# Kernel tuning notes

Hardware: AMD Instinct MI355X
Metric: run time of the kernel (lower is better)

## Reference

```python
import math
import jax, jax.numpy as jnp
import numpy as np

D_MODEL = 1024
D_STATE = 64
BATCH = 8
SEQLEN = 2048


def setup_inputs() -> dict:
    key = jax.random.key(0)
    ks = jax.random.split(key, 8)
    x = jax.random.normal(ks[0], (BATCH, SEQLEN, D_MODEL), dtype=jnp.float32)
    # faithful init: lam_real = -0.5 -> log_Lam_real = log(0.5); Lam_imag = pi*arange(N)
    log_Lam_real = jnp.log(0.5 * jnp.ones((D_STATE,), dtype=jnp.float32))
    Lam_imag = math.pi * jnp.arange(D_STATE, dtype=jnp.float32)
    B_real = 0.02 * jax.random.normal(ks[1], (D_STATE, D_MODEL), dtype=jnp.float32)
    B_imag = 0.02 * jax.random.normal(ks[2], (D_STATE, D_MODEL), dtype=jnp.float32)
    C_real = 0.02 * jax.random.normal(ks[3], (D_MODEL, D_STATE), dtype=jnp.float32)
    C_imag = 0.02 * jax.random.normal(ks[4], (D_MODEL, D_STATE), dtype=jnp.float32)
    Dp = jnp.ones((D_MODEL,), dtype=jnp.float32)
    log_dt = jnp.zeros((1,), dtype=jnp.float32)
    W_out = 0.02 * jax.random.normal(ks[5], (D_MODEL, D_MODEL), dtype=jnp.float32)
    b_out = jnp.zeros((D_MODEL,), dtype=jnp.float32)
    return {"x": x, "log_Lam_real": log_Lam_real, "Lam_imag": Lam_imag,
            "B_real": B_real, "B_imag": B_imag, "C_real": C_real, "C_imag": C_imag,
            "D": Dp, "log_dt": log_dt, "W_out": W_out, "b_out": b_out}


def reference(x, log_Lam_real, Lam_imag, B_real, B_imag, C_real, C_imag, D, log_dt, W_out, b_out):
    B, L, H = x.shape
    N = log_Lam_real.shape[0]
    dt = jnp.exp(log_dt)                          # (1,)
    Lam_r = -jnp.exp(log_Lam_real)                # (N,)
    mag = jnp.exp(Lam_r * dt)                     # (N,)
    Lbar_r = mag * jnp.cos(Lam_imag * dt)         # (N,)
    Lbar_i = mag * jnp.sin(Lam_imag * dt)         # (N,)
    # batched input projection for all timesteps: (B,L,N)
    Bu_r = jnp.einsum('blh,nh->bln', x, dt * B_real)
    Bu_i = jnp.einsum('blh,nh->bln', x, dt * B_imag)

    def step(carry, bu):
        sr, si = carry
        bur, bui = bu
        nr = Lbar_r * sr - Lbar_i * si + bur
        ni = Lbar_r * si + Lbar_i * sr + bui
        return (nr, ni), (nr, ni)

    sr0 = jnp.zeros((B, N), dtype=x.dtype)
    si0 = jnp.zeros((B, N), dtype=x.dtype)
    (sr, si), (SR, SI) = jax.lax.scan(
        step, (sr0, si0),
        (jnp.swapaxes(Bu_r, 0, 1), jnp.swapaxes(Bu_i, 0, 1)))  # scan over L; SR,SI: (L,B,N)
    # output: y_t = Re(C x_t) + D*u_t, vectorized over all t
    y = jnp.einsum('lbn,hn->blh', SR, C_real) - jnp.einsum('lbn,hn->blh', SI, C_imag) + D * x
    out = y @ W_out.T + b_out                     # out_proj (dropout is identity, p=0)
    return out, (sr, si)
```

## Files before the change

### kernel.cpp

```cpp
#include <hip/hip_runtime.h>

#define HD 1024
#define NS 64
#define NB 8
#define LS 2048
#define MT (NB*LS)
#define N2 128
#define KA 1152
#define CHL 16
#define NCH (LS/CHL)
#define NG  (NB*NS)

typedef __attribute__((ext_vector_type(8))) short short8;
typedef __attribute__((ext_vector_type(4))) float f32x4;

#define OB_ABUF 0u
#define OB_BMAT (OB_ABUF + MT*KA*2)
#define OB_BMP  (OB_BMAT + HD*KA*2)
#define OB_BU   (OB_BMP  + N2*HD*2)
#define OB_FR   (OB_BU   + MT*N2*4)
#define OB_FI   (OB_FR   + NG*NCH*4)
#define OB_CR   (OB_FI   + NG*NCH*4)
#define OB_CI   (OB_CR   + NG*NCH*4)
#define OB_WB   (OB_CI   + NG*NCH*4)
#define OB_CCT  (OB_WB   + HD*HD*2)

__device__ __forceinline__ unsigned short f2bf(float f) {
    unsigned u = __float_as_uint(f);
    u = (u + 0x7FFFu + ((u >> 16) & 1u)) >> 16;
    return (unsigned short)u;
}

__device__ __forceinline__ void lbar_of(int n, const float* __restrict__ logLr,
                                        const float* __restrict__ Li, float dt,
                                        float& ar, float& ai) {
    float lr  = -expf(logLr[n]);
    float mag = expf(lr * dt);
    float ang = Li[n] * dt;
    ar = mag * cosf(ang);
    ai = mag * sinf(ang);
}

__global__ __launch_bounds__(256) void k_prep(const float* __restrict__ x,
                                              const float* __restrict__ W,
                                              const float* __restrict__ Dv,
                                              const float* __restrict__ Br,
                                              const float* __restrict__ Bi,
                                              const float* __restrict__ Cr,
                                              const float* __restrict__ Ci,
                                              const float* __restrict__ log_dt,
                                              unsigned short* __restrict__ Ab,
                                              unsigned short* __restrict__ Bm,
                                              unsigned short* __restrict__ Bp,
                                              unsigned short* __restrict__ Wb,
                                              unsigned short* __restrict__ CCT) {
    __shared__ float T[64][65];
    const int blk = blockIdx.x;
    if (blk < 8192) {
        size_t idx = ((size_t)blk * 256 + threadIdx.x) * 8;
        int m = (int)(idx >> 10), k = (int)(idx & 1023);
        float4 v0 = *(const float4*)&x[idx];
        float4 v1 = *(const float4*)&x[idx + 4];
        short8 s;
        s[0]=f2bf(v0.x); s[1]=f2bf(v0.y); s[2]=f2bf(v0.z); s[3]=f2bf(v0.w);
        s[4]=f2bf(v1.x); s[5]=f2bf(v1.y); s[6]=f2bf(v1.z); s[7]=f2bf(v1.w);
        *(short8*)&Ab[(size_t)m * KA + k] = s;
    } else if (blk < 8704) {
        size_t idx = ((size_t)(blk - 8192) * 256 + threadIdx.x) * 8;
        int h = (int)(idx >> 10), k = (int)(idx & 1023);
        float4 v0 = *(const float4*)&W[idx];
        float4 v1 = *(const float4*)&W[idx + 4];
        float4 d0 = *(const float4*)&Dv[k];
        float4 d1 = *(const float4*)&Dv[k + 4];
        short8 s;
        s[0]=f2bf(v0.x*d0.x); s[1]=f2bf(v0.y*d0.y); s[2]=f2bf(v0.z*d0.z); s[3]=f2bf(v0.w*d0.w);
        s[4]=f2bf(v1.x*d1.x); s[5]=f2bf(v1.y*d1.y); s[6]=f2bf(v1.z*d1.z); s[7]=f2bf(v1.w*d1.w);
        *(short8*)&Bm[(size_t)h * KA + k] = s;
    } else if (blk < 8768) {
        size_t idx = ((size_t)(blk - 8704) * 256 + threadIdx.x) * 8;
        int n2 = (int)(idx >> 10), k = (int)(idx & 1023);
        float dt = expf(log_dt[0]);
        const float* src = (n2 < NS) ? &Br[(size_t)n2 * HD + k] : &Bi[(size_t)(n2 - NS) * HD + k];
        float4 v0 = *(const float4*)&src[0];
        float4 v1 = *(const float4*)&src[4];
        short8 s;
        s[0]=f2bf(v0.x*dt); s[1]=f2bf(v0.y*dt); s[2]=f2bf(v0.z*dt); s[3]=f2bf(v0.w*dt);
        s[4]=f2bf(v1.x*dt); s[5]=f2bf(v1.y*dt); s[6]=f2bf(v1.z*dt); s[7]=f2bf(v1.w*dt);
        *(short8*)&Bp[(size_t)n2 * HD + k] = s;
    } else if (blk < 9280) {
        size_t idx = ((size_t)(blk - 8768) * 256 + threadIdx.x) * 8;
        float4 v0 = *(const float4*)&W[idx];
        float4 v1 = *(const float4*)&W[idx + 4];
        short8 s;
        s[0]=f2bf(v0.x); s[1]=f2bf(v0.y); s[2]=f2bf(v0.z); s[3]=f2bf(v0.w);
        s[4]=f2bf(v1.x); s[5]=f2bf(v1.y); s[6]=f2bf(v1.z); s[7]=f2bf(v1.w);
        *(short8*)&Wb[idx] = s;
    } else {
        const int local = blk - 9280;
        const int h0 = (local & 15) * 64;
        const int half = local >> 4;
        const float* src = half ? Ci : Cr;
        const float sgn = half ? -1.f : 1.f;
        const int tid = threadIdx.x;
        const int j = tid & 63, i4 = tid >> 6;
        #pragma unroll
        for (int p = 0; p < 16; ++p) {
            int i = p * 4 + i4;
            T[i][j] = src[(size_t)(h0 + i) * NS + j];
        }
        __syncthreads();
        #pragma unroll
        for (int p = 0; p < 16; ++p) {
            int jj = p * 4 + i4;
            CCT[(size_t)(half * NS + jj) * HD + h0 + j] = f2bf(sgn * T[j][jj]);
        }
    }
}

__global__ __launch_bounds__(256) void k_carry(const float* __restrict__ Bu,
                                               const float* __restrict__ logLr,
                                               const float* __restrict__ Li,
                                               const float* __restrict__ log_dt,
                                               float* __restrict__ Fr,
                                               float* __restrict__ Fi) {
    int g = blockIdx.x * 256 + threadIdx.x;
    int n = g & 63, ch = (g >> 6) & (NCH - 1), b = g >> 13;
    float dt = expf(log_dt[0]);
    float ar, ai; lbar_of(n, logLr, Li, dt, ar, ai);
    float sr = 0.f, si = 0.f;
    size_t base = ((size_t)b * LS + ch * CHL) * N2;
    #pragma unroll 4
    for (int j = 0; j < CHL; ++j) {
        float ur = Bu[base + j * N2 + n];
        float ui = Bu[base + j * N2 + NS + n];
        float nr = ar * sr - ai * si + ur;
        float ni = ar * si + ai * sr + ui;
        sr = nr; si = ni;
    }
    int fi = ch * NG + b * 64 + n;
    Fr[fi] = sr; Fi[fi] = si;
}

__global__ __launch_bounds__(256) void k_scan2(const float* __restrict__ Fr,
                                               const float* __restrict__ Fi,
                                               const float* __restrict__ logLr,
                                               const float* __restrict__ Li,
                                               const float* __restrict__ log_dt,
                                               float* __restrict__ CexR,
                                               float* __restrict__ CexI,
                                               float* __restrict__ out_tail) {
    int g = blockIdx.x * 256 + threadIdx.x;
    if (g >= NG) return;
    int n = g & 63;
    float dt = expf(log_dt[0]);
    float ar, ai; lbar_of(n, logLr, Li, dt, ar, ai);
    float Ar = ar, Ai = ai;
    #pragma unroll
    for (int s = 0; s < 4; ++s) { float nr = Ar*Ar - Ai*Ai; Ai = 2.f*Ar*Ai; Ar = nr; }
    float cr = 0.f, ci = 0.f;
    for (int ch = 0; ch < NCH; ++ch) {
        CexR[ch * NG + g] = cr; CexI[ch * NG + g] = ci;
        float fr = Fr[ch * NG + g], fi2 = Fi[ch * NG + g];
        float nr = Ar * cr - Ai * ci + fr;
        float ni = Ar * ci + Ai * cr + fi2;
        cr = nr; ci = ni;
    }
    out_tail[g]       = cr;
    out_tail[NG + g]  = ci;
}

__global__ __launch_bounds__(256) void k_scan3(const float* __restrict__ Bu,
                                               const float* __restrict__ CexR,
                                               const float* __restrict__ CexI,
                                               const float* __restrict__ logLr,
                                               const float* __restrict__ Li,
                                               const float* __restrict__ log_dt,
                                               unsigned short* __restrict__ Ab) {
    int g = blockIdx.x * 256 + threadIdx.x;
    int n = g & 63, ch = (g >> 6) & (NCH - 1), b = g >> 13;
    float dt = expf(log_dt[0]);
    float ar, ai; lbar_of(n, logLr, Li, dt, ar, ai);
    int ci_idx = ch * NG + b * 64 + n;
    float sr = CexR[ci_idx], si = CexI[ci_idx];
    size_t base = ((size_t)b * LS + ch * CHL);
    #pragma unroll 4
    for (int j = 0; j < CHL; ++j) {
        size_t m = base + j;
        float ur = Bu[m * N2 + n];
        float ui = Bu[m * N2 + NS + n];
        float nr = ar * sr - ai * si + ur;
        float ni = ar * si + ai * sr + ui;
        sr = nr; si = ni;
        Ab[m * KA + HD + n]      = f2bf(sr);
        Ab[m * KA + HD + NS + n] = f2bf(si);
    }
}

template<int KTOT>
__device__ __forceinline__ void gemm_body(const unsigned short* __restrict__ A, int lda,
                                          const unsigned short* __restrict__ B, int ldb,
                                          const float* __restrict__ bias, int has_bias,
                                          void* __restrict__ outp, int ldo, int bf16out,
                                          int m0, int n0) {
    constexpr int T = KTOT / 32;
    __shared__ unsigned short At[3][128 * 32];
    __shared__ unsigned short Bt[3][128 * 32];
    const int tid = threadIdx.x, wv = tid >> 6, ln = tid & 63;
    const int wr = wv >> 1, wc = wv & 1;
    const int r16 = ln & 15, kg = ln >> 4;
    f32x4 zero = {0.f, 0.f, 0.f, 0.f};
    f32x4 acc[4][4];
    #pragma unroll
    for (int i = 0; i < 4; ++i)
        #pragma unroll
        for (int j = 0; j < 4; ++j) acc[i][j] = zero;

    auto STAGE = [&](int t, int s) {
        const int kt = t * 32;
        #pragma unroll
        for (int i = 0; i < 2; ++i) {
            int e = i * 4096 + wv * 1024 + ln * 16;
            int row = e >> 6, kb = e & 63;
            const char* ga = (const char*)A + ((size_t)(m0 + row) * lda + kt) * 2 + kb;
            __builtin_amdgcn_global_load_lds(
                (const __attribute__((address_space(1))) void*)ga,
                (__attribute__((address_space(3))) void*)((char*)At[s] + i * 4096 + wv * 1024),
                16, 0, 0);
            const char* gb = (const char*)B + ((size_t)(n0 + row) * ldb + kt) * 2 + kb;
            __builtin_amdgcn_global_load_lds(
                (const __attribute__((address_space(1))) void*)gb,
                (__attribute__((address_space(3))) void*)((char*)Bt[s] + i * 4096 + wv * 1024),
                16, 0, 0);
        }
    };

    STAGE(0, 0); STAGE(1, 1); STAGE(2, 2);
    int s = 0;
    for (int t = 0; t < T; ++t) {
        if (t + 2 < T)      asm volatile("s_waitcnt vmcnt(8)" ::: "memory");
        else if (t + 1 < T) asm volatile("s_waitcnt vmcnt(4)" ::: "memory");
        else                asm volatile("s_waitcnt vmcnt(0)" ::: "memory");
        __builtin_amdgcn_s_barrier();
        asm volatile("" ::: "memory");
        short8 af[4], bfr[4];
        #pragma unroll
        for (int i = 0; i < 4; ++i) {
            af[i]  = *(const short8*)&At[s][(wr * 64 + i * 16 + r16) * 32 + kg * 8];
            bfr[i] = *(const short8*)&Bt[s][(wc * 64 + i * 16 + r16) * 32 + kg * 8];
        }
        __builtin_amdgcn_s_setprio(1);
        #pragma unroll
        for (int i = 0; i < 4; ++i)
            #pragma unroll
            for (int j = 0; j < 4; ++j)
                acc[i][j] = __builtin_amdgcn_mfma_f32_16x16x32_bf16(af[i], bfr[j], acc[i][j], 0, 0, 0);
        __builtin_amdgcn_s_setprio(0);
        asm volatile("" ::: "memory");
        __builtin_amdgcn_s_barrier();
        if (t + 3 < T) STAGE(t + 3, s);
        if (++s == 3) s = 0;
    }
    #pragma unroll
    for (int j = 0; j < 4; ++j) {
        int col = n0 + wc * 64 + j * 16 + r16;
        float bv = has_bias ? bias[col] : 0.f;
        #pragma unroll
        for (int i = 0; i < 4; ++i) {
            #pragma unroll
            for (int r = 0; r < 4; ++r) {
                int row = m0 + wr * 64 + i * 16 + kg * 4 + r;
                if (bf16out) ((unsigned short*)outp)[(size_t)row * ldo + col] = f2bf(acc[i][j][r] + bv);
                else         ((float*)outp)[(size_t)row * ldo + col] = acc[i][j][r] + bv;
            }
        }
    }
}

__global__ __launch_bounds__(256) void k_gemm_big(const unsigned short* __restrict__ A,
                                                  const unsigned short* __restrict__ B,
                                                  const float* __restrict__ bias,
                                                  float* __restrict__ out) {
    gemm_body<KA>(A, KA, B, KA, bias, 1, out, HD, 0, blockIdx.x * 128, blockIdx.y * 128);
}

__global__ __launch_bounds__(256) void k_gemm_small(const unsigned short* __restrict__ Abuf,
                                                    const unsigned short* __restrict__ Bmp,
                                                    const unsigned short* __restrict__ Wb,
                                                    const unsigned short* __restrict__ CCT,
                                                    float* __restrict__ Bu,
                                                    unsigned short* __restrict__ BmE2) {
    const int bx = blockIdx.x;
    if (bx < 128) {
        gemm_body<1024>(Abuf, KA, Bmp, 1024, nullptr, 0, Bu, 128, 0, bx * 128, 0);
    } else {
        gemm_body<1024>(Wb, 1024, CCT, 1024, nullptr, 0, BmE2, KA, 1, (bx - 128) * 128, 0);
    }
}

extern "C" void kernel_launch(void* const* d_in, const int* in_sizes, int n_in,
                              void* d_out, int out_size, void* d_ws, size_t ws_size,
                              hipStream_t stream) {
    const float* x      = (const float*)d_in[0];
    const float* logLr  = (const float*)d_in[1];
    const float* Li     = (const float*)d_in[2];
    const float* Br     = (const float*)d_in[3];
    const float* Bi     = (const float*)d_in[4];
    const float* Cr     = (const float*)d_in[5];
    const float* Ci     = (const float*)d_in[6];
    const float* Dv     = (const float*)d_in[7];
    const float* log_dt = (const float*)d_in[8];
    const float* W      = (const float*)d_in[9];
    const float* bo     = (const float*)d_in[10];
    float* out = (float*)d_out;
    char*  ws  = (char*)d_ws;

    unsigned short* Abuf = (unsigned short*)(ws + OB_ABUF);
    unsigned short* Bmat = (unsigned short*)(ws + OB_BMAT);
    unsigned short* Bmp  = (unsigned short*)(ws + OB_BMP);
    float* Bu   = (float*)(ws + OB_BU);
    float* Fr   = (float*)(ws + OB_FR);
    float* Fi   = (float*)(ws + OB_FI);
    float* CexR = (float*)(ws + OB_CR);
    float* CexI = (float*)(ws + OB_CI);
    unsigned short* Wb   = (unsigned short*)(ws + OB_WB);
    unsigned short* CCT  = (unsigned short*)(ws + OB_CCT);

    k_prep <<<9312, 256, 0, stream>>>(x, W, Dv, Br, Bi, Cr, Ci, log_dt, Abuf, Bmat, Bmp, Wb, CCT);
    k_gemm_small<<<136, 256, 0, stream>>>(Abuf, Bmp, Wb, CCT, Bu, Bmat + HD);
    k_carry<<<(NB * NS * NCH) / 256, 256, 0, stream>>>(Bu, logLr, Li, log_dt, Fr, Fi);
    k_scan2<<<2, 256, 0, stream>>>(Fr, Fi, logLr, Li, log_dt, CexR, CexI, out + (size_t)MT * HD);
    k_scan3<<<(NB * NS * NCH) / 256, 256, 0, stream>>>(Bu, CexR, CexI, logLr, Li, log_dt, Abuf);
    k_gemm_big<<<dim3(MT / 128, HD / 128), 256, 0, stream>>>(Abuf, Bmat, bo, out);
}
```

Measured before the change: 234.0 us.

## Fuse chunk carry into small GEMM, warp-parallel carry scan, simplify big GEMM

The per-chunk carry computation runs inside the small-GEMM blocks right after each block writes its Bu tile. This removes the separate k_carry launch and a re-read of Bu from a fresh kernel. The 128-step serial cross-chunk scan becomes a wavefront shuffle-based parallel prefix scan of affine complex maps, one wave per state-batch pair. Separately, the big output GEMM drops its 3-stage global_load_lds ring and s_setprio for a single-buffer load/sync/compute loop. That frees LDS but loses the overlap of loads with MFMA in the dominant kernel.

```diff
diff --git a/kernel.cpp b/kernel.cpp
--- a/kernel.cpp
+++ b/kernel.cpp
@@ -117,56 +117,168 @@
     }
 }
 
-__global__ __launch_bounds__(256) void k_carry(const float* __restrict__ Bu,
-                                               const float* __restrict__ logLr,
-                                               const float* __restrict__ Li,
-                                               const float* __restrict__ log_dt,
-                                               float* __restrict__ Fr,
-                                               float* __restrict__ Fi) {
-    int g = blockIdx.x * 256 + threadIdx.x;
-    int n = g & 63, ch = (g >> 6) & (NCH - 1), b = g >> 13;
-    float dt = expf(log_dt[0]);
-    float ar, ai; lbar_of(n, logLr, Li, dt, ar, ai);
-    float sr = 0.f, si = 0.f;
-    size_t base = ((size_t)b * LS + ch * CHL) * N2;
-    #pragma unroll 4
-    for (int j = 0; j < CHL; ++j) {
-        float ur = Bu[base + j * N2 + n];
-        float ui = Bu[base + j * N2 + NS + n];
-        float nr = ar * sr - ai * si + ur;
-        float ni = ar * si + ai * sr + ui;
-        sr = nr; si = ni;
-    }
-    int fi = ch * NG + b * 64 + n;
-    Fr[fi] = sr; Fi[fi] = si;
-}
-
-__global__ __launch_bounds__(256) void k_scan2(const float* __restrict__ Fr,
-                                               const float* __restrict__ Fi,
-                                               const float* __restrict__ logLr,
-                                               const float* __restrict__ Li,
-                                               const float* __restrict__ log_dt,
-                                               float* __restrict__ CexR,
-                                               float* __restrict__ CexI,
-                                               float* __restrict__ out_tail) {
-    int g = blockIdx.x * 256 + threadIdx.x;
-    if (g >= NG) return;
-    int n = g & 63;
-    float dt = expf(log_dt[0]);
+template<int KTOT>
+__device__ __forceinline__ void gemm_ring(const unsigned short* __restrict__ A, int lda,
+                                          const unsigned short* __restrict__ B, int ldb,
+                                          void* __restrict__ outp, int ldo, int bf16out,
+                                          int m0, int n0,
+                                          unsigned short* At_base, unsigned short* Bt_base) {
+    constexpr int T = KTOT / 32;
+    const int tid = threadIdx.x, wv = tid >> 6, ln = tid & 63;
+    const int wr = wv >> 1, wc = wv & 1;
+    const int r16 = ln & 15, kg = ln >> 4;
+    f32x4 zero = {0.f, 0.f, 0.f, 0.f};
+    f32x4 acc[4][4];
+    #pragma unroll
+    for (int i = 0; i < 4; ++i)
+        #pragma unroll
+        for (int j = 0; j < 4; ++j) acc[i][j] = zero;
+
+    auto STAGE = [&](int t, int s) {
+        const int kt = t * 32;
+        #pragma unroll
+        for (int i = 0; i < 2; ++i) {
+            int e = i * 4096 + wv * 1024 + ln * 16;
+            int row = e >> 6, kb = e & 63;
+            const char* ga = (const char*)A + ((size_t)(m0 + row) * lda + kt) * 2 + kb;
+            __builtin_amdgcn_global_load_lds(
+                (const __attribute__((address_space(1))) void*)ga,
+                (__attribute__((address_space(3))) void*)((char*)At_base + s * 8192 + i * 4096 + wv * 1024),
+                16, 0, 0);
+            const char* gb = (const char*)B + ((size_t)(n0 + row) * ldb + kt) * 2 + kb;
+            __builtin_amdgcn_global_load_lds(
+                (const __attribute__((address_space(1))) void*)gb,
+                (__attribute__((address_space(3))) void*)((char*)Bt_base + s * 8192 + i * 4096 + wv * 1024),
+                16, 0, 0);
+        }
+    };
+
+    STAGE(0, 0); STAGE(1, 1); STAGE(2, 2);
+    int s = 0;
+    for (int t = 0; t < T; ++t) {
+        if (t + 2 < T)      asm volatile("s_waitcnt vmcnt(8)" ::: "memory");
+        else if (t + 1 < T) asm volatile("s_waitcnt vmcnt(4)" ::: "memory");
+        else                asm volatile("s_waitcnt vmcnt(0)" ::: "memory");
+        __builtin_amdgcn_s_barrier();
+        asm volatile("" ::: "memory");
+        short8 af[4], bfr[4];
+        #pragma unroll
+        for (int i = 0; i < 4; ++i) {
+            af[i]  = *(const short8*)&At_base[s * 4096 + (wr * 64 + i * 16 + r16) * 32 + kg * 8];
+            bfr[i] = *(const short8*)&Bt_base[s * 4096 + (wc * 64 + i * 16 + r16) * 32 + kg * 8];
+        }
+        __builtin_amdgcn_s_setprio(1);
+        #pragma unroll
+        for (int i = 0; i < 4; ++i)
+            #pragma unroll
+            for (int j = 0; j < 4; ++j)
+                acc[i][j] = __builtin_amdgcn_mfma_f32_16x16x32_bf16(af[i], bfr[j], acc[i][j], 0, 0, 0);
+        __builtin_amdgcn_s_setprio(0);
+        asm volatile("" ::: "memory");
+        __builtin_amdgcn_s_barrier();
+        if (t + 3 < T) STAGE(t + 3, s);
+        if (++s == 3) s = 0;
+    }
+    #pragma unroll
+    for (int j = 0; j < 4; ++j) {
+        int col = n0 + wc * 64 + j * 16 + r16;
+        #pragma unroll
+        for (int i = 0; i < 4; ++i) {
+            #pragma unroll
+            for (int r = 0; r < 4; ++r) {
+                int row = m0 + wr * 64 + i * 16 + kg * 4 + r;
+                if (bf16out) ((unsigned short*)outp)[(size_t)row * ldo + col] = f2bf(acc[i][j][r]);
+                else         ((float*)outp)[(size_t)row * ldo + col] = acc[i][j][r];
+            }
+        }
+    }
+}
+
+__global__ __launch_bounds__(256) void k_gemm_small(const unsigned short* __restrict__ Abuf,
+                                                    const unsigned short* __restrict__ Bmp,
+                                                    const unsigned short* __restrict__ Wb,
+                                                    const unsigned short* __restrict__ CCT,
+                                                    float* __restrict__ Bu,
+                                                    unsigned short* __restrict__ BmE2,
+                                                    const float* __restrict__ logLr,
+                                                    const float* __restrict__ Li,
+                                                    const float* __restrict__ log_dt,
+                                                    float* __restrict__ Fr,
+                                                    float* __restrict__ Fi) {
+    __shared__ unsigned short At[3 * 128 * 32];
+    __shared__ unsigned short Bt[3 * 128 * 32];
+    const int bx = blockIdx.x;
+    if (bx < 128) {
+        const int m0 = bx * 128;
+        gemm_ring<1024>(Abuf, KA, Bmp, 1024, Bu, 128, 0, m0, 0, At, Bt);
+        __syncthreads();
+        const int b = m0 >> 11, lch0 = (m0 & 2047) >> 4;
+        const float dt = expf(log_dt[0]);
+        #pragma unroll
+        for (int w = 0; w < 2; ++w) {
+            int item = w * 256 + threadIdx.x;
+            int ch_l = item >> 6, n = item & 63;
+            float ar, ai; lbar_of(n, logLr, Li, dt, ar, ai);
+            float sr = 0.f, si = 0.f;
+            size_t base = ((size_t)m0 + ch_l * CHL) * N2;
+            #pragma unroll 4
+            for (int j = 0; j < CHL; ++j) {
+                float ur = Bu[base + j * N2 + n];
+                float ui = Bu[base + j * N2 + NS + n];
+                float nr = ar * sr - ai * si + ur;
+                float ni = ar * si + ai * sr + ui;
+                sr = nr; si = ni;
+            }
+            int fi = (lch0 + ch_l) * NG + b * 64 + n;
+            Fr[fi] = sr; Fi[fi] = si;
+        }
+    } else {
+        gemm_ring<1024>(Wb, 1024, CCT, 1024, BmE2, KA, 1, (bx - 128) * 128, 0, At, Bt);
+    }
+}
+
+__global__ __launch_bounds__(512) void k_scan2w(const float* __restrict__ Fr,
+                                                const float* __restrict__ Fi,
+                                                const float* __restrict__ logLr,
+                                                const float* __restrict__ Li,
+                                                const float* __restrict__ log_dt,
+                                                float* __restrict__ CexR,
+                                                float* __restrict__ CexI,
+                                                float* __restrict__ out_tail) {
+    const int wv = threadIdx.x >> 6, l = threadIdx.x & 63;
+    const int g = blockIdx.x * 8 + wv;
+    const int n = g & 63;
+    const float dt = expf(log_dt[0]);
     float ar, ai; lbar_of(n, logLr, Li, dt, ar, ai);
     float Ar = ar, Ai = ai;
     #pragma unroll
     for (int s = 0; s < 4; ++s) { float nr = Ar*Ar - Ai*Ai; Ai = 2.f*Ar*Ai; Ar = nr; }
-    float cr = 0.f, ci = 0.f;
-    for (int ch = 0; ch < NCH; ++ch) {
-        CexR[ch * NG + g] = cr; CexI[ch * NG + g] = ci;
-        float fr = Fr[ch * NG + g], fi2 = Fi[ch * NG + g];
-        float nr = Ar * cr - Ai * ci + fr;
-        float ni = Ar * ci + Ai * cr + fi2;
-        cr = nr; ci = ni;
-    }
-    out_tail[g]       = cr;
-    out_tail[NG + g]  = ci;
+    const int ch0 = 2 * l;
+    float f0r = Fr[ch0 * NG + g],       f0i = Fi[ch0 * NG + g];
+    float f1r = Fr[(ch0 + 1) * NG + g], f1i = Fi[(ch0 + 1) * NG + g];
+    float qar = Ar*Ar - Ai*Ai,           qai = 2.f*Ar*Ai;
+    float qbr = Ar*f0r - Ai*f0i + f1r,   qbi = Ar*f0i + Ai*f0r + f1i;
+    #pragma unroll
+    for (int d = 1; d < 64; d <<= 1) {
+        float par = __shfl_up(qar, d, 64);
+        float pai = __shfl_up(qai, d, 64);
+        float pbr = __shfl_up(qbr, d, 64);
+        float pbi = __shfl_up(qbi, d, 64);
+        if (l >= d) {
+            float nar = qar*par - qai*pai;
+            float nai = qar*pai + qai*par;
+            float nbr = qar*pbr - qai*pbi + qbr;
+            float nbi = qar*pbi + qai*pbr + qbi;
+            qar = nar; qai = nai; qbr = nbr; qbi = nbi;
+        }
+    }
+    float ebr = __shfl_up(qbr, 1, 64);
+    float ebi = __shfl_up(qbi, 1, 64);
+    if (l == 0) { ebr = 0.f; ebi = 0.f; }
+    CexR[ch0 * NG + g] = ebr;  CexI[ch0 * NG + g] = ebi;
+    CexR[(ch0 + 1) * NG + g] = Ar*ebr - Ai*ebi + f0r;
+    CexI[(ch0 + 1) * NG + g] = Ar*ebi + Ai*ebr + f0i;
+    if (l == 63) { out_tail[g] = qbr; out_tail[NG + g] = qbi; }
 }
 
 __global__ __launch_bounds__(256) void k_scan3(const float* __restrict__ Bu,
@@ -196,15 +308,13 @@
     }
 }
 
-template<int KTOT>
-__device__ __forceinline__ void gemm_body(const unsigned short* __restrict__ A, int lda,
-                                          const unsigned short* __restrict__ B, int ldb,
-                                          const float* __restrict__ bias, int has_bias,
-                                          void* __restrict__ outp, int ldo, int bf16out,
-                                          int m0, int n0) {
-    constexpr int T = KTOT / 32;
-    __shared__ unsigned short At[3][128 * 32];
-    __shared__ unsigned short Bt[3][128 * 32];
+__global__ __launch_bounds__(256) void k_gemm_big(const unsigned short* __restrict__ A,
+                                                  const unsigned short* __restrict__ B,
+                                                  const float* __restrict__ bias,
+                                                  float* __restrict__ out) {
+    __shared__ unsigned short At[128 * 32];
+    __shared__ unsigned short Bt[128 * 32];
+    const int m0 = blockIdx.x * 128, n0 = blockIdx.y * 128;
     const int tid = threadIdx.x, wv = tid >> 6, ln = tid & 63;
     const int wr = wv >> 1, wc = wv & 1;
     const int r16 = ln & 15, kg = ln >> 4;
@@ -215,85 +325,48 @@
         #pragma unroll
         for (int j = 0; j < 4; ++j) acc[i][j] = zero;
 
-    auto STAGE = [&](int t, int s) {
-        const int kt = t * 32;
+    for (int kt = 0; kt < KA; kt += 32) {
         #pragma unroll
         for (int i = 0; i < 2; ++i) {
             int e = i * 4096 + wv * 1024 + ln * 16;
             int row = e >> 6, kb = e & 63;
-            const char* ga = (const char*)A + ((size_t)(m0 + row) * lda + kt) * 2 + kb;
+            const char* ga = (const char*)A + ((size_t)(m0 + row) * KA + kt) * 2 + kb;
             __builtin_amdgcn_global_load_lds(
                 (const __attribute__((address_space(1))) void*)ga,
-                (__attribute__((address_space(3))) void*)((char*)At[s] + i * 4096 + wv * 1024),
+                (__attribute__((address_space(3))) void*)((char*)At + i * 4096 + wv * 1024),
                 16, 0, 0);
-            const char* gb = (const char*)B + ((size_t)(n0 + row) * ldb + kt) * 2 + kb;
+            const char* gb = (const char*)B + ((size_t)(n0 + row) * KA + kt) * 2 + kb;
             __builtin_amdgcn_global_load_lds(
                 (const __attribute__((address_space(1))) void*)gb,
-                (__attribute__((address_space(3))) void*)((char*)Bt[s] + i * 4096 + wv * 1024),
+                (__attribute__((address_space(3))) void*)((char*)Bt + i * 4096 + wv * 1024),
                 16, 0, 0);
         }
-    };
-
-    STAGE(0, 0); STAGE(1, 1); STAGE(2, 2);
-    int s = 0;
-    for (int t = 0; t < T; ++t) {
-        if (t + 2 < T)      asm volatile("s_waitcnt vmcnt(8)" ::: "memory");
-        else if (t + 1 < T) asm volatile("s_waitcnt vmcnt(4)" ::: "memory");
-        else                asm volatile("s_waitcnt vmcnt(0)" ::: "memory");
-        __builtin_amdgcn_s_barrier();
-        asm volatile("" ::: "memory");
+        __syncthreads();
         short8 af[4], bfr[4];
         #pragma unroll
         for (int i = 0; i < 4; ++i) {
-            af[i]  = *(const short8*)&At[s][(wr * 64 + i * 16 + r16) * 32 + kg * 8];
-            bfr[i] = *(const short8*)&Bt[s][(wc * 64 + i * 16 + r16) * 32 + kg * 8];
-        }
-        __builtin_amdgcn_s_setprio(1);
+            af[i]  = *(const short8*)&At[(wr * 64 + i * 16 + r16) * 32 + kg * 8];
+            bfr[i] = *(const short8*)&Bt[(wc * 64 + i * 16 + r16) * 32 + kg * 8];
+        }
         #pragma unroll
         for (int i = 0; i < 4; ++i)
             #pragma unroll
             for (int j = 0; j < 4; ++j)
                 acc[i][j] = __builtin_amdgcn_mfma_f32_16x16x32_bf16(af[i], bfr[j], acc[i][j], 0, 0, 0);
-        __builtin_amdgcn_s_setprio(0);
-        asm volatile("" ::: "memory");
-        __builtin_amdgcn_s_barrier();
-        if (t + 3 < T) STAGE(t + 3, s);
-        if (++s == 3) s = 0;
+        __syncthreads();
     }
     #pragma unroll
     for (int j = 0; j < 4; ++j) {
         int col = n0 + wc * 64 + j * 16 + r16;
-        float bv = has_bias ? bias[col] : 0.f;
+        float bv = bias[col];
         #pragma unroll
         for (int i = 0; i < 4; ++i) {
             #pragma unroll
             for (int r = 0; r < 4; ++r) {
                 int row = m0 + wr * 64 + i * 16 + kg * 4 + r;
-                if (bf16out) ((unsigned short*)outp)[(size_t)row * ldo + col] = f2bf(acc[i][j][r] + bv);
-                else         ((float*)outp)[(size_t)row * ldo + col] = acc[i][j][r] + bv;
+                out[(size_t)row * HD + col] = acc[i][j][r] + bv;
             }
         }
-    }
-}
-
-__global__ __launch_bounds__(256) void k_gemm_big(const unsigned short* __restrict__ A,
-                                                  const unsigned short* __restrict__ B,
-                                                  const float* __restrict__ bias,
-                                                  float* __restrict__ out) {
-    gemm_body<KA>(A, KA, B, KA, bias, 1, out, HD, 0, blockIdx.x * 128, blockIdx.y * 128);
-}
-
-__global__ __launch_bounds__(256) void k_gemm_small(const unsigned short* __restrict__ Abuf,
-                                                    const unsigned short* __restrict__ Bmp,
-                                                    const unsigned short* __restrict__ Wb,
-                                                    const unsigned short* __restrict__ CCT,
-                                                    float* __restrict__ Bu,
-                                                    unsigned short* __restrict__ BmE2) {
-    const int bx = blockIdx.x;
-    if (bx < 128) {
-        gemm_body<1024>(Abuf, KA, Bmp, 1024, nullptr, 0, Bu, 128, 0, bx * 128, 0);
-    } else {
-        gemm_body<1024>(Wb, 1024, CCT, 1024, nullptr, 0, BmE2, KA, 1, (bx - 128) * 128, 0);
     }
 }
 
@@ -326,9 +399,9 @@
     unsigned short* CCT  = (unsigned short*)(ws + OB_CCT);
 
     k_prep <<<9312, 256, 0, stream>>>(x, W, Dv, Br, Bi, Cr, Ci, log_dt, Abuf, Bmat, Bmp, Wb, CCT);
-    k_gemm_small<<<136, 256, 0, stream>>>(Abuf, Bmp, Wb, CCT, Bu, Bmat + HD);
-    k_carry<<<(NB * NS * NCH) / 256, 256, 0, stream>>>(Bu, logLr, Li, log_dt, Fr, Fi);
-    k_scan2<<<2, 256, 0, stream>>>(Fr, Fi, logLr, Li, log_dt, CexR, CexI, out + (size_t)MT * HD);
+    k_gemm_small<<<136, 256, 0, stream>>>(Abuf, Bmp, Wb, CCT, Bu, Bmat + HD,
+                                          logLr, Li, log_dt, Fr, Fi);
+    k_scan2w<<<64, 512, 0, stream>>>(Fr, Fi, logLr, Li, log_dt, CexR, CexI, out + (size_t)MT * HD);
     k_scan3<<<(NB * NS * NCH) / 256, 256, 0, stream>>>(Bu, CexR, CexI, logLr, Li, log_dt, Abuf);
     k_gemm_big<<<dim3(MT / 128, HD / 128), 256, 0, stream>>>(Abuf, Bmat, bo, out);
 }
```

Result: no change. 230.0 us (-1.7%).
